# Optimization experiments

Hardware: AMD Instinct MI355X
Metric: run time of the kernel (lower is better)

## Reference

```python
import jax, jax.numpy as jnp
import numpy as np

N = 32768       # tokens
D_IN = 1024     # input_dim
D_OUT = 1024    # output_dim
E = 8           # num_experts
TOP_K = 2


def setup_inputs() -> dict:
    key = jax.random.key(0)
    k1, k2, k3, k4, k5 = jax.random.split(key, 5)
    scale = 1.0 / np.sqrt(D_IN)
    return {
        "x": jax.random.normal(k1, (N, D_IN), dtype=jnp.float32),
        "Wg": jax.random.uniform(k2, (E, D_IN), jnp.float32, -scale, scale),
        "bg": jax.random.uniform(k3, (E,), jnp.float32, -scale, scale),
        "W": jax.random.uniform(k4, (E, D_OUT, D_IN), jnp.float32, -scale, scale),
        "b": jax.random.uniform(k5, (E, D_OUT), jnp.float32, -scale, scale),
    }


def reference(x, Wg, bg, W, b):
    # Gating: softmax over experts, then top-k (weights NOT renormalized,
    # matching the original module).
    gate_scores = x @ Wg.T + bg                      # [N, E]
    gate_probs = jax.nn.softmax(gate_scores, axis=-1)
    topk_w, topk_idx = jax.lax.top_k(gate_probs, TOP_K)  # [N, K]

    # Per-token combine weight for each expert: sum_k w_k * onehot(idx_k)
    combine = (jax.nn.one_hot(topk_idx, E, dtype=x.dtype)
               * topk_w[..., None]).sum(axis=1)      # [N, E]

    # Dense per-expert GEMM + weighted combine (loop over small fixed E).
    out = jnp.zeros((x.shape[0], D_OUT), dtype=x.dtype)
    for e in range(E):
        out = out + combine[:, e:e + 1] * (x @ W[e].T + b[e])
    return out
```

## Files before the change

kernel.cpp:

```cpp
#include <hip/hip_runtime.h>
#include <hip/hip_bf16.h>
#include <cstdint>
#include <cstddef>

#define N_TOK   32768
#define D_IN    1024
#define D_OUT   1024
#define NE      8

typedef __attribute__((ext_vector_type(4))) float floatx4;
typedef __attribute__((ext_vector_type(8))) short bf16x8;

__device__ __forceinline__ unsigned short f2bf(float f) {
  union { float f; unsigned int u; } v; v.f = f;
  unsigned int u = v.u + 0x7fffu + ((v.u >> 16) & 1u);
  return (unsigned short)(u >> 16);
}

__device__ __forceinline__ unsigned short f2h(float f) {
  union { _Float16 hf; unsigned short us; } c; c.hf = (_Float16)f; return c.us;
}
__device__ __forceinline__ float h2f(unsigned short u) {
  union { _Float16 hf; unsigned short us; } c; c.us = u; return (float)c.hf;
}

__device__ __forceinline__ void gload_lds16(const void* g, void* l) {
  __builtin_amdgcn_global_load_lds(
      (const __attribute__((address_space(1))) unsigned int*)g,
      (__attribute__((address_space(3))) unsigned int*)l, 16, 0, 0);
}

__global__ __launch_bounds__(256) void prep_kernel(
    const float* __restrict__ x,
    const float* __restrict__ Wg,
    const float* __restrict__ bg,
    const float* __restrict__ W,
    unsigned short* __restrict__ xb,
    unsigned short* __restrict__ Wb,
    int* __restrict__ counts,
    int* __restrict__ bids,
    float* __restrict__ bw,
    int* __restrict__ tok2slot,
    float* __restrict__ out,
    int zero_out)
{
  __shared__ float wg_lds[NE * D_IN];
  __shared__ int lcnt[NE];
  __shared__ int basee[NE];
  __shared__ int   tok_e[64][2];
  __shared__ int   tok_s[64][2];
  __shared__ float tok_w[64][2];

  const int blk = blockIdx.x;
  const int tid = threadIdx.x;

  if (blk >= 1024) {
    if (!zero_out) return;
    float4* o4 = (float4*)out;
    const int base = (blk - 1024) * 4096;
#pragma unroll
    for (int i = 0; i < 16; ++i)
      o4[base + i * 256 + tid] = (float4){0.f, 0.f, 0.f, 0.f};
    return;
  }
  if (blk >= 512) {
    const float4* s = (const float4*)W;
    const int base = (blk - 512) * 4096;
#pragma unroll
    for (int i = 0; i < 16; ++i) {
      int idx = base + i * 256 + tid;
      float4 v = s[idx];
      ushort4 h;
      h.x = f2bf(v.x); h.y = f2bf(v.y); h.z = f2bf(v.z); h.w = f2bf(v.w);
      ((ushort4*)Wb)[idx] = h;
    }
    return;
  }

  {
    const float4* s = (const float4*)Wg;
    float4* d = (float4*)wg_lds;
    for (int i = tid; i < NE * D_IN / 4; i += 256) d[i] = s[i];
  }
  if (tid < NE) lcnt[tid] = 0;
  __syncthreads();

  const int wave = tid >> 6, lane = tid & 63;
  const float4* x4 = (const float4*)x;
  const float4* w4 = (const float4*)wg_lds;

  for (int t = 0; t < 16; ++t) {
    const int lt = wave * 16 + t;
    const int n  = blk * 64 + lt;
    float4 xv[4];
    float acc[NE];
#pragma unroll
    for (int e = 0; e < NE; ++e) acc[e] = 0.f;
#pragma unroll
    for (int j = 0; j < 4; ++j) {
      xv[j] = x4[(size_t)n * 256 + j * 64 + lane];
#pragma unroll
      for (int e = 0; e < NE; ++e) {
        float4 w = w4[e * 256 + j * 64 + lane];
        acc[e] += xv[j].x * w.x + xv[j].y * w.y + xv[j].z * w.z + xv[j].w * w.w;
      }
    }
#pragma unroll
    for (int j = 0; j < 4; ++j) {
      ushort4 h;
      h.x = f2bf(xv[j].x); h.y = f2bf(xv[j].y);
      h.z = f2bf(xv[j].z); h.w = f2bf(xv[j].w);
      ((ushort4*)xb)[(size_t)n * 256 + j * 64 + lane] = h;
    }
#pragma unroll
    for (int e = 0; e < NE; ++e)
#pragma unroll
      for (int s = 32; s > 0; s >>= 1)
        acc[e] += __shfl_xor(acc[e], s, 64);

    if (lane == 0) {
      float sc[NE];
#pragma unroll
      for (int e = 0; e < NE; ++e) sc[e] = acc[e] + bg[e];
      float m = sc[0];
#pragma unroll
      for (int e = 1; e < NE; ++e) m = fmaxf(m, sc[e]);
      float p[NE], den = 0.f;
#pragma unroll
      for (int e = 0; e < NE; ++e) { p[e] = __expf(sc[e] - m); den += p[e]; }
      int e1 = 0;
#pragma unroll
      for (int e = 1; e < NE; ++e) if (sc[e] > sc[e1]) e1 = e;
      int e2 = (e1 == 0) ? 1 : 0;
#pragma unroll
      for (int e = 0; e < NE; ++e) if (e != e1 && sc[e] > sc[e2]) e2 = e;
      float inv = 1.f / den;
      tok_e[lt][0] = e1; tok_w[lt][0] = p[e1] * inv; tok_s[lt][0] = atomicAdd(&lcnt[e1], 1);
      tok_e[lt][1] = e2; tok_w[lt][1] = p[e2] * inv; tok_s[lt][1] = atomicAdd(&lcnt[e2], 1);
    }
  }
  __syncthreads();
  if (tid < NE) basee[tid] = atomicAdd(&counts[tid], lcnt[tid]);
  __syncthreads();
  if (tid < 128) {
    int lt = tid >> 1, kk = tid & 1;
    int e = tok_e[lt][kk];
    int slot = basee[e] + tok_s[lt][kk];
    int token = blk * 64 + lt;
    bids[e * N_TOK + slot] = token;
    bw[e * N_TOK + slot]   = tok_w[lt][kk];
    tok2slot[token * 2 + kk] = (e << 15) | slot;
  }
}

__global__ __launch_bounds__(256) void moe_gemm_kernel(
    const unsigned short* __restrict__ xb,
    const unsigned short* __restrict__ Wb,
    const float* __restrict__ bias,
    const int* __restrict__ counts,
    const int* __restrict__ bids,
    const float* __restrict__ bw,
    float* __restrict__ out,
    void* __restrict__ y,
    int mode)
{
  const int bid = blockIdx.x;
  const int e   = bid & 7;
  const int nt  = (bid >> 3) & 7;
  const int mt  = bid >> 6;
  const int cnt = counts[e];
  const int row0 = mt << 7;
  if (row0 >= cnt) return;
  const int rows = min(128, cnt - row0);

  __shared__ alignas(16) unsigned short Ald[128 * 32];
  __shared__ alignas(16) unsigned short Bld[128 * 32];
  __shared__ int   ids[128];
  __shared__ float wts[128];

  const int tid = threadIdx.x;
  if (tid < 128) {
    int src = (tid < rows) ? tid : 0;
    ids[tid] = bids[e * N_TOK + row0 + src];
    wts[tid] = (tid < rows) ? bw[e * N_TOK + row0 + tid] : 0.f;
  }
  __syncthreads();

  const int wave = tid >> 6;
  const int lane = tid & 63;
  const int wm = wave >> 1, wn = wave & 1;

  const int srow = lane >> 2;
  const int koff = (lane & 3) * 8;
  const int seg  = wave * 32;
  const long a_r0 = (long)ids[seg + srow] * D_IN;
  const long a_r1 = (long)ids[seg + 16 + srow] * D_IN;
  const unsigned short* wbe = Wb + (size_t)e * D_OUT * D_IN;
  const long b_r0 = (long)(nt * 128 + seg + srow) * D_IN;
  const long b_r1 = (long)(nt * 128 + seg + 16 + srow) * D_IN;
  unsigned short* aL0 = &Ald[seg * 32];
  unsigned short* aL1 = &Ald[(seg + 16) * 32];
  unsigned short* bL0 = &Bld[seg * 32];
  unsigned short* bL1 = &Bld[(seg + 16) * 32];

  const int m16  = lane & 15;
  const int quad = lane >> 4;

  floatx4 acc[4][4];
#pragma unroll
  for (int i = 0; i < 4; ++i)
#pragma unroll
    for (int j = 0; j < 4; ++j) acc[i][j] = (floatx4){0.f, 0.f, 0.f, 0.f};

  for (int k0 = 0; k0 < D_IN; k0 += 32) {
    gload_lds16(xb + a_r0 + k0 + koff, aL0);
    gload_lds16(xb + a_r1 + k0 + koff, aL1);
    gload_lds16(wbe + b_r0 + k0 + koff, bL0);
    gload_lds16(wbe + b_r1 + k0 + koff, bL1);
    __syncthreads();

    bf16x8 af[4], bf[4];
#pragma unroll
    for (int i = 0; i < 4; ++i)
      af[i] = *(const bf16x8*)&Ald[(wm * 64 + i * 16 + m16) * 32 + quad * 8];
#pragma unroll
    for (int j = 0; j < 4; ++j)
      bf[j] = *(const bf16x8*)&Bld[(wn * 64 + j * 16 + m16) * 32 + quad * 8];
#pragma unroll
    for (int i = 0; i < 4; ++i)
#pragma unroll
      for (int j = 0; j < 4; ++j)
        acc[i][j] = __builtin_amdgcn_mfma_f32_16x16x32_bf16(af[i], bf[j], acc[i][j], 0, 0, 0);
    __syncthreads();
  }

  float bv[4];
  int col[4];
#pragma unroll
  for (int j = 0; j < 4; ++j) {
    col[j] = nt * 128 + wn * 64 + j * 16 + m16;
    bv[j] = bias[e * D_OUT + col[j]];
  }

  int ybase = 0;
  if (mode) {
#pragma unroll
    for (int i = 0; i < NE; ++i) ybase += (i < e) ? counts[i] : 0;
  }

#pragma unroll
  for (int i = 0; i < 4; ++i) {
#pragma unroll
    for (int r = 0; r < 4; ++r) {
      int rl = wm * 64 + i * 16 + quad * 4 + r;
      if (rl < rows) {
        float w = wts[rl];
        if (mode == 0) {
          float* orow = out + (size_t)ids[rl] * D_OUT;
#pragma unroll
          for (int j = 0; j < 4; ++j)
            atomicAdd(&orow[col[j]], w * (acc[i][j][r] + bv[j]));
        } else if (mode == 2) {
          float* yrow = (float*)y + (size_t)(ybase + row0 + rl) * D_OUT;
#pragma unroll
          for (int j = 0; j < 4; ++j)
            yrow[col[j]] = w * (acc[i][j][r] + bv[j]);
        } else {
          unsigned short* yrow = (unsigned short*)y + (size_t)(ybase + row0 + rl) * D_OUT;
#pragma unroll
          for (int j = 0; j < 4; ++j)
            yrow[col[j]] = f2h(w * (acc[i][j][r] + bv[j]));
        }
      }
    }
  }
}

__global__ __launch_bounds__(256) void combine_kernel(
    const void* __restrict__ y,
    const int* __restrict__ counts,
    const int* __restrict__ tok2slot,
    float* __restrict__ out,
    int mode)
{
  __shared__ int pre[NE];
  if (threadIdx.x < NE) {
    int s = 0;
    for (int i = 0; i < threadIdx.x; ++i) s += counts[i];
    pre[threadIdx.x] = s;
  }
  __syncthreads();

  const int total = N_TOK * (D_OUT / 4);
  for (int idx = blockIdx.x * 256 + threadIdx.x; idx < total; idx += 2048 * 256) {
    int row = idx >> 8, c4 = idx & 255;
    int v1 = tok2slot[row * 2], v2 = tok2slot[row * 2 + 1];
    long r1 = pre[v1 >> 15] + (v1 & 32767);
    long r2 = pre[v2 >> 15] + (v2 & 32767);
    float4 o;
    if (mode == 2) {
      const float4* y4 = (const float4*)y;
      float4 a = y4[r1 * 256 + c4];
      float4 b = y4[r2 * 256 + c4];
      o.x = a.x + b.x; o.y = a.y + b.y; o.z = a.z + b.z; o.w = a.w + b.w;
    } else {
      const ushort4* y4 = (const ushort4*)y;
      ushort4 a = y4[r1 * 256 + c4];
      ushort4 b = y4[r2 * 256 + c4];
      o.x = h2f(a.x) + h2f(b.x); o.y = h2f(a.y) + h2f(b.y);
      o.z = h2f(a.z) + h2f(b.z); o.w = h2f(a.w) + h2f(b.w);
    }
    ((float4*)out)[idx] = o;
  }
}

extern "C" void kernel_launch(void* const* d_in, const int* in_sizes, int n_in,
                              void* d_out, int out_size, void* d_ws, size_t ws_size,
                              hipStream_t stream) {
  const float* x  = (const float*)d_in[0];
  const float* Wg = (const float*)d_in[1];
  const float* bg = (const float*)d_in[2];
  const float* W  = (const float*)d_in[3];
  const float* b  = (const float*)d_in[4];
  float* out = (float*)d_out;

  char* ws = (char*)d_ws;
  size_t off = 0;
  int*   counts   = (int*)(ws + off);  off += 4096;
  int*   bids     = (int*)(ws + off);  off += (size_t)NE * N_TOK * 4;
  float* bw       = (float*)(ws + off); off += (size_t)NE * N_TOK * 4;
  int*   tok2slot = (int*)(ws + off);  off += (size_t)N_TOK * 2 * 4;
  unsigned short* xb = (unsigned short*)(ws + off); off += (size_t)N_TOK * D_IN * 2;
  unsigned short* Wb = (unsigned short*)(ws + off); off += (size_t)NE * D_IN * D_OUT * 2;
  void* y = (void*)(ws + off);
  const size_t y_rows = 2 * (size_t)N_TOK;
  const size_t need_f32 = off + y_rows * D_OUT * 4;
  const size_t need_f16 = off + y_rows * D_OUT * 2;

  int mode = (ws_size >= need_f32) ? 2 : (ws_size >= need_f16 ? 1 : 0);

  hipMemsetAsync(counts, 0, NE * sizeof(int), stream);
  prep_kernel<<<3072, 256, 0, stream>>>(x, Wg, bg, W, xb, Wb, counts, bids, bw,
                                        tok2slot, out, mode == 0 ? 1 : 0);
  moe_gemm_kernel<<<NE * 256 * 8, 256, 0, stream>>>(xb, Wb, b, counts, bids, bw,
                                                    out, y, mode);
  if (mode != 0)
    combine_kernel<<<2048, 256, 0, stream>>>(y, counts, tok2slot, out, mode);
}
```

Baseline: 543.9 us.

## Enlarge MoE GEMM tile to 256x256 with triple-buffered LDS pipeline

The grouped expert GEMM moves from 128x128 tiles with 256 threads to 256x256 tiles with 512 threads. It adds a three-stage LDS ring buffer that prefetches two K-tiles ahead with explicit vmcnt waits and raw barriers, an XOR swizzle to avoid LDS bank conflicts, and setprio around the MFMA bursts. The goals are better operand reuse per tile, overlap of global loads with compute, and one barrier fewer per K-step. It also shrinks the prep kernel grid when the atomic output path is not used. In exchange it raises register pressure from 128 accumulators per thread and increases LDS use, which may limit occupancy.

```diff
diff --git a/kernel.cpp b/kernel.cpp
--- a/kernel.cpp
+++ b/kernel.cpp
@@ -7,6 +7,11 @@
 #define D_IN    1024
 #define D_OUT   1024
 #define NE      8
+
+#define BM 256
+#define BN 256
+#define BK 32
+#define NTILES (D_IN / BK)
 
 typedef __attribute__((ext_vector_type(4))) float floatx4;
 typedef __attribute__((ext_vector_type(8))) short bf16x8;
@@ -153,7 +158,7 @@
   }
 }
 
-__global__ __launch_bounds__(256) void moe_gemm_kernel(
+__global__ __launch_bounds__(512, 2) void moe_gemm_kernel(
     const unsigned short* __restrict__ xb,
     const unsigned short* __restrict__ Wb,
     const float* __restrict__ bias,
@@ -166,79 +171,115 @@
 {
   const int bid = blockIdx.x;
   const int e   = bid & 7;
-  const int nt  = (bid >> 3) & 7;
-  const int mt  = bid >> 6;
+  const int nt  = (bid >> 3) & 3;
+  const int mt  = bid >> 5;
   const int cnt = counts[e];
-  const int row0 = mt << 7;
+  const int row0 = mt << 8;
   if (row0 >= cnt) return;
-  const int rows = min(128, cnt - row0);
-
-  __shared__ alignas(16) unsigned short Ald[128 * 32];
-  __shared__ alignas(16) unsigned short Bld[128 * 32];
-  __shared__ int   ids[128];
-  __shared__ float wts[128];
+  const int rows = min(BM, cnt - row0);
+
+  __shared__ alignas(16) unsigned short Ald[3][BM * BK];
+  __shared__ alignas(16) unsigned short Bld[3][BN * BK];
+  __shared__ int   ids[BM];
+  __shared__ float wts[BM];
 
   const int tid = threadIdx.x;
-  if (tid < 128) {
+  if (tid < BM) {
     int src = (tid < rows) ? tid : 0;
     ids[tid] = bids[e * N_TOK + row0 + src];
     wts[tid] = (tid < rows) ? bw[e * N_TOK + row0 + tid] : 0.f;
   }
   __syncthreads();
 
-  const int wave = tid >> 6;
+  const int w    = tid >> 6;
   const int lane = tid & 63;
-  const int wm = wave >> 1, wn = wave & 1;
-
-  const int srow = lane >> 2;
-  const int koff = (lane & 3) * 8;
-  const int seg  = wave * 32;
-  const long a_r0 = (long)ids[seg + srow] * D_IN;
-  const long a_r1 = (long)ids[seg + 16 + srow] * D_IN;
-  const unsigned short* wbe = Wb + (size_t)e * D_OUT * D_IN;
-  const long b_r0 = (long)(nt * 128 + seg + srow) * D_IN;
-  const long b_r1 = (long)(nt * 128 + seg + 16 + srow) * D_IN;
-  unsigned short* aL0 = &Ald[seg * 32];
-  unsigned short* aL1 = &Ald[(seg + 16) * 32];
-  unsigned short* bL0 = &Bld[seg * 32];
-  unsigned short* bL1 = &Bld[(seg + 16) * 32];
-
+  const int wm   = w >> 2;
+  const int wn   = w & 3;
   const int m16  = lane & 15;
   const int quad = lane >> 4;
 
-  floatx4 acc[4][4];
-#pragma unroll
-  for (int i = 0; i < 4; ++i)
+  const unsigned short* wbe = Wb + (size_t)e * D_OUT * D_IN;
+
+  size_t a_goff[2], b_goff[2];
+  int ldsgrp[2];
+#pragma unroll
+  for (int i2 = 0; i2 < 2; ++i2) {
+    const int g = w * 2 + i2;
+    const int r = g * 16 + (lane >> 2);
+    const int c = (lane & 3) ^ ((r >> 1) & 3);
+    a_goff[i2] = (size_t)ids[r] * D_IN + c * 8;
+    b_goff[i2] = (size_t)(nt * BN + r) * D_IN + c * 8;
+    ldsgrp[i2] = g * 512;
+  }
+
+  const int swz  = (quad ^ ((m16 >> 1) & 3)) * 8;
+  const int roff = m16 * BK + swz;
+
+  floatx4 acc[8][4];
+#pragma unroll
+  for (int i = 0; i < 8; ++i)
 #pragma unroll
     for (int j = 0; j < 4; ++j) acc[i][j] = (floatx4){0.f, 0.f, 0.f, 0.f};
 
-  for (int k0 = 0; k0 < D_IN; k0 += 32) {
-    gload_lds16(xb + a_r0 + k0 + koff, aL0);
-    gload_lds16(xb + a_r1 + k0 + koff, aL1);
-    gload_lds16(wbe + b_r0 + k0 + koff, bL0);
-    gload_lds16(wbe + b_r1 + k0 + koff, bL1);
-    __syncthreads();
-
-    bf16x8 af[4], bf[4];
+#pragma unroll
+  for (int t0 = 0; t0 < 2; ++t0) {
+    const int kb = t0 * BK;
+#pragma unroll
+    for (int i2 = 0; i2 < 2; ++i2) {
+      gload_lds16(xb  + a_goff[i2] + kb, &Ald[t0][ldsgrp[i2]]);
+      gload_lds16(wbe + b_goff[i2] + kb, &Bld[t0][ldsgrp[i2]]);
+    }
+  }
+
+  int rcur = 0, rnxt = 2;
+  for (int t = 0; t < NTILES; ++t) {
+    const int kb2 = (t + 2 < NTILES ? t + 2 : NTILES - 1) * BK;
+    gload_lds16(xb + a_goff[0] + kb2, &Ald[rnxt][ldsgrp[0]]);
+    gload_lds16(xb + a_goff[1] + kb2, &Ald[rnxt][ldsgrp[1]]);
+    asm volatile("s_waitcnt vmcnt(6)" ::: "memory");
+    __builtin_amdgcn_s_barrier();
+    asm volatile("" ::: "memory");
+
+    bf16x8 bf[4], af[4];
+#pragma unroll
+    for (int j = 0; j < 4; ++j)
+      bf[j] = *(const bf16x8*)&Bld[rcur][(wn * 64 + j * 16) * BK + roff];
 #pragma unroll
     for (int i = 0; i < 4; ++i)
-      af[i] = *(const bf16x8*)&Ald[(wm * 64 + i * 16 + m16) * 32 + quad * 8];
-#pragma unroll
-    for (int j = 0; j < 4; ++j)
-      bf[j] = *(const bf16x8*)&Bld[(wn * 64 + j * 16 + m16) * 32 + quad * 8];
+      af[i] = *(const bf16x8*)&Ald[rcur][(wm * 128 + i * 16) * BK + roff];
+    __builtin_amdgcn_s_setprio(1);
 #pragma unroll
     for (int i = 0; i < 4; ++i)
 #pragma unroll
       for (int j = 0; j < 4; ++j)
         acc[i][j] = __builtin_amdgcn_mfma_f32_16x16x32_bf16(af[i], bf[j], acc[i][j], 0, 0, 0);
-    __syncthreads();
+    __builtin_amdgcn_s_setprio(0);
+
+    gload_lds16(wbe + b_goff[0] + kb2, &Bld[rnxt][ldsgrp[0]]);
+    gload_lds16(wbe + b_goff[1] + kb2, &Bld[rnxt][ldsgrp[1]]);
+#pragma unroll
+    for (int i = 0; i < 4; ++i)
+      af[i] = *(const bf16x8*)&Ald[rcur][(wm * 128 + 64 + i * 16) * BK + roff];
+    __builtin_amdgcn_s_setprio(1);
+#pragma unroll
+    for (int i = 0; i < 4; ++i)
+#pragma unroll
+      for (int j = 0; j < 4; ++j)
+        acc[i + 4][j] = __builtin_amdgcn_mfma_f32_16x16x32_bf16(af[i], bf[j], acc[i + 4][j], 0, 0, 0);
+    __builtin_amdgcn_s_setprio(0);
+
+    asm volatile("" ::: "memory");
+    __builtin_amdgcn_s_barrier();
+    asm volatile("" ::: "memory");
+    rcur = (rcur == 2) ? 0 : rcur + 1;
+    rnxt = (rnxt == 2) ? 0 : rnxt + 1;
   }
 
   float bv[4];
   int col[4];
 #pragma unroll
   for (int j = 0; j < 4; ++j) {
-    col[j] = nt * 128 + wn * 64 + j * 16 + m16;
+    col[j] = nt * BN + wn * 64 + j * 16 + m16;
     bv[j] = bias[e * D_OUT + col[j]];
   }
 
@@ -249,27 +290,27 @@
   }
 
 #pragma unroll
-  for (int i = 0; i < 4; ++i) {
+  for (int i = 0; i < 8; ++i) {
 #pragma unroll
     for (int r = 0; r < 4; ++r) {
-      int rl = wm * 64 + i * 16 + quad * 4 + r;
+      int rl = wm * 128 + i * 16 + quad * 4 + r;
       if (rl < rows) {
-        float w = wts[rl];
+        float wgt = wts[rl];
         if (mode == 0) {
           float* orow = out + (size_t)ids[rl] * D_OUT;
 #pragma unroll
           for (int j = 0; j < 4; ++j)
-            atomicAdd(&orow[col[j]], w * (acc[i][j][r] + bv[j]));
+            atomicAdd(&orow[col[j]], wgt * (acc[i][j][r] + bv[j]));
         } else if (mode == 2) {
           float* yrow = (float*)y + (size_t)(ybase + row0 + rl) * D_OUT;
 #pragma unroll
           for (int j = 0; j < 4; ++j)
-            yrow[col[j]] = w * (acc[i][j][r] + bv[j]);
+            yrow[col[j]] = wgt * (acc[i][j][r] + bv[j]);
         } else {
           unsigned short* yrow = (unsigned short*)y + (size_t)(ybase + row0 + rl) * D_OUT;
 #pragma unroll
           for (int j = 0; j < 4; ++j)
-            yrow[col[j]] = f2h(w * (acc[i][j][r] + bv[j]));
+            yrow[col[j]] = f2h(wgt * (acc[i][j][r] + bv[j]));
         }
       }
     }
@@ -340,10 +381,10 @@
   int mode = (ws_size >= need_f32) ? 2 : (ws_size >= need_f16 ? 1 : 0);
 
   hipMemsetAsync(counts, 0, NE * sizeof(int), stream);
-  prep_kernel<<<3072, 256, 0, stream>>>(x, Wg, bg, W, xb, Wb, counts, bids, bw,
-                                        tok2slot, out, mode == 0 ? 1 : 0);
-  moe_gemm_kernel<<<NE * 256 * 8, 256, 0, stream>>>(xb, Wb, b, counts, bids, bw,
-                                                    out, y, mode);
+  prep_kernel<<<mode == 0 ? 3072 : 1024, 256, 0, stream>>>(
+      x, Wg, bg, W, xb, Wb, counts, bids, bw, tok2slot, out, mode == 0 ? 1 : 0);
+  moe_gemm_kernel<<<NE * 4 * (N_TOK / BM), 512, 0, stream>>>(
+      xb, Wb, b, counts, bids, bw, out, y, mode);
   if (mode != 0)
     combine_kernel<<<2048, 256, 0, stream>>>(y, counts, tok2slot, out, mode);
 }
```

Measured after the change: 567.9 us. +4.4%, slower.
